# Optimization experiments

Hardware: AMD Instinct MI355X
Metric: run time of the kernel (lower is better)

The kernel has to match this reference:

```python
import jax, jax.numpy as jnp
import numpy as np
import math

V, D, L, M, S, B = 32000, 1024, 4, 4096, 2048, 4


def sinusoidal_positional_encoding(max_seq_len, embedding_dim):
    position = jnp.arange(max_seq_len, dtype=jnp.float32)[:, None]
    div_term = jnp.exp(jnp.arange(0, embedding_dim, 2, dtype=jnp.float32)
                       * (-math.log(10000.0) / embedding_dim))
    pe = jnp.zeros((max_seq_len, embedding_dim), jnp.float32)
    pe = pe.at[:, 0::2].set(jnp.sin(position * div_term))
    pe = pe.at[:, 1::2].set(jnp.cos(position * div_term))
    return pe


def setup_inputs() -> dict:
    key = jax.random.key(0)
    ks = jax.random.split(key, 12)
    s = 0.02
    return {
        "x": jax.random.randint(ks[0], (B, S), 0, V, dtype=jnp.int64),
        "emb": jax.random.normal(ks[1], (V, D), jnp.float32) * s,
        "pos_enc": sinusoidal_positional_encoding(S, D),
        "wq": jax.random.normal(ks[2], (D, D), jnp.float32) * s,
        "bq": jnp.zeros((D,), jnp.float32),
        "wk": jax.random.normal(ks[3], (D, D), jnp.float32) * s,
        "bk": jnp.zeros((D,), jnp.float32),
        "wv": jax.random.normal(ks[4], (D, D), jnp.float32) * s,
        "bv": jnp.zeros((D,), jnp.float32),
        "w1s": jax.random.normal(ks[5], (L, D, M), jnp.float32) * s,
        "b1s": jnp.zeros((L, M), jnp.float32),
        "w2s": jax.random.normal(ks[6], (L, M, D), jnp.float32) * s,
        "b2s": jnp.zeros((L, D), jnp.float32),
    }


def reference(x, emb, pos_enc, wq, bq, wk, bk, wv, bv, w1s, b1s, w2s, b2s):
    seq = x.shape[1]
    h = emb[x] + pos_enc[:seq]                      # [B,S,D]
    q = h @ wq + bq
    k = h @ wk + bk
    v = h @ wv + bv
    scores = jnp.einsum('bqd,bkd->bqk', q, k) / jnp.sqrt(jnp.float32(k.shape[-1]))
    # Faithful to source: triu(diagonal=0) KEPT -> attends to self and future.
    mask = jnp.triu(jnp.ones((seq, seq), bool), k=0)
    scores = jnp.where(mask, scores, -jnp.inf)
    attn = jax.nn.softmax(scores, axis=-1)
    h = jax.nn.relu(jnp.einsum('bqk,bkd->bqd', attn, v))
    for i in range(w1s.shape[0]):
        h = jax.nn.relu(h @ w1s[i] + b1s[i])
        h = jax.nn.relu(h @ w2s[i] + b2s[i])
    return h
```

## Files before the change

### kernel.cpp

```cpp
#include <hip/hip_runtime.h>

#define D_DIM 1024
#define S_DIM 2048
#define B_DIM 4
#define M_DIM 4096
#define NTOK  8192

typedef unsigned short u16;
typedef __attribute__((ext_vector_type(8))) short short8;
typedef __attribute__((ext_vector_type(4))) float fx4;

static __device__ __forceinline__ float b2f(u16 u) {
  union { unsigned int i; float f; } v; v.i = ((unsigned int)u) << 16; return v.f;
}
static __device__ __forceinline__ u16 f2b(float f) {
  union { float f; unsigned int i; } v; v.f = f;
  unsigned int r = v.i + 0x7fffu + ((v.i >> 16) & 1u);
  return (u16)(r >> 16);
}
static __device__ __forceinline__ void async16(u16* lds, const u16* g) {
  __builtin_amdgcn_global_load_lds(
      (__attribute__((address_space(1))) void*)(u16*)g,
      (__attribute__((address_space(3))) void*)lds, 16, 0, 0);
}

__global__ void canary_kernel(float* __restrict__ out) {
  const long i = ((long)blockIdx.x * 256 + threadIdx.x) * 4;
  float4 v = {1.0f, 1.0f, 1.0f, 1.0f};
  *(float4*)(out + i) = v;
}

__global__ void Transformer_33792802685820_kernel(
    const int* __restrict__ x, const float* __restrict__ emb,
    const float* __restrict__ pe, u16* __restrict__ h) {
  const int t = blockIdx.x;
  const int s = t & (S_DIM - 1);
  const int row = x[t];
  const int d = threadIdx.x * 4;
  float4 e = *(const float4*)(emb + (long)row * D_DIM + d);
  float4 p = *(const float4*)(pe + (long)s * D_DIM + d);
  ushort4 o;
  o.x = f2b(e.x + p.x);
  o.y = f2b(e.y + p.y);
  o.z = f2b(e.z + p.z);
  o.w = f2b(e.w + p.w);
  *(ushort4*)(h + (long)t * D_DIM + d) = o;
}

__global__ void transpose_f_kernel(
    const float* __restrict__ in, u16* __restrict__ out, int R, int C) {
  __shared__ float tile[32][33];
  const int c0 = blockIdx.x * 32, r0 = blockIdx.y * 32;
  const int tx = threadIdx.x, ty = threadIdx.y;
  for (int i = ty; i < 32; i += 8)
    tile[i][tx] = in[(long)(r0 + i) * C + (c0 + tx)];
  __syncthreads();
  for (int i = ty; i < 32; i += 8)
    out[(long)(c0 + i) * R + (r0 + tx)] = f2b(tile[tx][i]);
}

__global__ void transpose_b_kernel(
    const u16* __restrict__ in, u16* __restrict__ out, int R, int C) {
  __shared__ u16 tile[32][33];
  const long zoff = (long)blockIdx.z * R * C;
  const int c0 = blockIdx.x * 32, r0 = blockIdx.y * 32;
  const int tx = threadIdx.x, ty = threadIdx.y;
  for (int i = ty; i < 32; i += 8)
    tile[i][tx] = in[zoff + (long)(r0 + i) * C + (c0 + tx)];
  __syncthreads();
  for (int i = ty; i < 32; i += 8)
    out[zoff + (long)(c0 + i) * R + (r0 + tx)] = tile[tx][i];
}

template<int BN, bool RELU, bool BIAS, bool OUTF32>
__global__ __launch_bounds__(512) void gemm256(
    const u16* __restrict__ A, const u16* __restrict__ Bt,
    const float* __restrict__ bias, u16* __restrict__ C, float* __restrict__ Cf,
    int M, int N, int K, float scale, long sA_, long sB_, long sC_) {
  static_assert(BN == 256 || BN == 128, "BN");
  constexpr int WN   = BN / 64;
  constexpr int WM   = 8 / WN;
  constexpr int MF   = 256 / (WM * 16);
  constexpr int NB_B = BN / 64;

  __shared__ u16 sA0[256 * 64];
  __shared__ u16 sA1[256 * 64];
  __shared__ u16 sB0[BN * 64];
  __shared__ u16 sB1[BN * 64];

  const int tid  = threadIdx.x;
  const int lane = tid & 63;
  const int wave = tid >> 6;
  const int quad = lane >> 4;
  const int l16  = lane & 15;
  const int wm   = wave / WN;
  const int wn   = wave % WN;

  const int gx  = gridDim.x;
  const int nwg = gx * gridDim.y;
  const int id0 = blockIdx.y * gx + blockIdx.x;
  const int cpx = nwg >> 3;
  const int sid = (id0 & 7) * cpx + (id0 >> 3);
  const int n0  = (sid % gx) * BN;
  const int m0  = (sid / gx) << 8;

  A  += (long)blockIdx.z * sA_;
  Bt += (long)blockIdx.z * sB_;

  const int srow = tid >> 3;
  const int pc   = tid & 7;
  const int lc   = pc ^ (srow & 7);
  const u16* gA0 = A  + (long)(m0 + srow) * K + lc * 8;
  const u16* gB0 = Bt + (long)(n0 + srow) * K + lc * 8;
  const int ldst = tid << 3;

  fx4 acc[MF][4] = {};

  const int NT = K >> 6;

#define STG(Sa, Sb, t) do { \
    const long ko_ = (long)(t) << 6; \
    _Pragma("unroll") for (int bb_ = 0; bb_ < 4; ++bb_) \
      async16(&Sa[bb_ * 4096 + ldst], gA0 + (long)(bb_ * 64) * K + ko_); \
    _Pragma("unroll") for (int bb_ = 0; bb_ < NB_B; ++bb_) \
      async16(&Sb[bb_ * 4096 + ldst], gB0 + (long)(bb_ * 64) * K + ko_); \
  } while (0)

#define HALF(Sa, Sb) do { \
    _Pragma("unroll") for (int ks_ = 0; ks_ < 2; ++ks_) { \
      const int cko_ = ((((ks_) << 2) | quad) ^ (l16 & 7)) << 3; \
      short8 ar_[MF], br_[4]; \
      _Pragma("unroll") for (int i_ = 0; i_ < MF; ++i_) { \
        const int r_ = wm * (MF * 16) + i_ * 16 + l16; \
        ar_[i_] = *(const short8*)&Sa[(r_ >> 6) * 4096 + (r_ & 63) * 64 + cko_]; \
      } \
      _Pragma("unroll") for (int n_ = 0; n_ < 4; ++n_) { \
        const int r_ = wn * 64 + n_ * 16 + l16; \
        br_[n_] = *(const short8*)&Sb[(r_ >> 6) * 4096 + (r_ & 63) * 64 + cko_]; \
      } \
      __builtin_amdgcn_s_setprio(1); \
      _Pragma("unroll") for (int i_ = 0; i_ < MF; ++i_) \
        _Pragma("unroll") for (int n_ = 0; n_ < 4; ++n_) \
          acc[i_][n_] = __builtin_amdgcn_mfma_f32_16x16x32_bf16( \
              ar_[i_], br_[n_], acc[i_][n_], 0, 0, 0); \
      __builtin_amdgcn_s_setprio(0); \
    } \
  } while (0)

#define TILE_END do { \
    __builtin_amdgcn_sched_barrier(0); \
    asm volatile("s_waitcnt vmcnt(0)"); \
    __builtin_amdgcn_s_barrier(); \
    __builtin_amdgcn_sched_barrier(0); \
  } while (0)

  STG(sA0, sB0, 0);
  TILE_END;

  for (int t = 0; t < NT; t += 2) {
    STG(sA1, sB1, t + 1);
    HALF(sA0, sB0);
    TILE_END;
    if (t + 2 < NT) STG(sA0, sB0, t + 2);
    HALF(sA1, sB1);
    TILE_END;
  }

  float bv[4];
  #pragma unroll
  for (int n = 0; n < 4; ++n)
    bv[n] = BIAS ? bias[n0 + wn * 64 + n * 16 + l16] : 0.0f;

  #pragma unroll
  for (int f = 0; f < MF; ++f) {
    #pragma unroll
    for (int r = 0; r < 4; ++r) {
      const long row  = m0 + wm * (MF * 16) + f * 16 + quad * 4 + r;
      const long base = (long)blockIdx.z * sC_ + row * N + n0 + wn * 64 + l16;
      #pragma unroll
      for (int n = 0; n < 4; ++n) {
        float v = acc[f][n][r] * scale + bv[n];
        if (RELU) { if (v < 0.0f) v = 0.0f; }
        if (OUTF32) Cf[base + n * 16] = v;
        else        C [base + n * 16] = f2b(v);
      }
    }
  }
#undef STG
#undef HALF
#undef TILE_END
}

__global__ void softmax_kernel(u16* __restrict__ P) {
  const int q = blockIdx.x;
  u16* p = P + ((long)blockIdx.y * S_DIM + q) * S_DIM;
  const int tid = threadIdx.x;
  const int wave = tid >> 6, lane = tid & 63;
  __shared__ float red[4];
  float vals[8];
  float mx = -3.0e38f;
  for (int it = 0; it < 8; ++it) {
    int k = tid + it * 256;
    float v = (k >= q) ? b2f(p[k]) : -3.0e38f;
    vals[it] = v;
    mx = fmaxf(mx, v);
  }
  for (int off = 32; off > 0; off >>= 1)
    mx = fmaxf(mx, __shfl_down(mx, off, 64));
  if (lane == 0) red[wave] = mx;
  __syncthreads();
  mx = fmaxf(fmaxf(red[0], red[1]), fmaxf(red[2], red[3]));
  __syncthreads();
  float sum = 0.0f;
  for (int it = 0; it < 8; ++it) {
    int k = tid + it * 256;
    float e = (k >= q) ? __expf(vals[it] - mx) : 0.0f;
    vals[it] = e;
    sum += e;
  }
  for (int off = 32; off > 0; off >>= 1)
    sum += __shfl_down(sum, off, 64);
  if (lane == 0) red[wave] = sum;
  __syncthreads();
  sum = red[0] + red[1] + red[2] + red[3];
  const float inv = 1.0f / sum;
  for (int it = 0; it < 8; ++it) {
    int k = tid + it * 256;
    p[k] = f2b(vals[it] * inv);
  }
}

extern "C" void kernel_launch(void* const* d_in, const int* in_sizes, int n_in,
                              void* d_out, int out_size, void* d_ws, size_t ws_size,
                              hipStream_t stream) {
  (void)in_sizes; (void)n_in; (void)out_size; (void)ws_size;
  const int*   x   = (const int*)d_in[0];
  const float* emb = (const float*)d_in[1];
  const float* pe  = (const float*)d_in[2];
  const float* wq  = (const float*)d_in[3];
  const float* bq  = (const float*)d_in[4];
  const float* wk  = (const float*)d_in[5];
  const float* bk  = (const float*)d_in[6];
  const float* wv  = (const float*)d_in[7];
  const float* bv  = (const float*)d_in[8];
  const float* w1s = (const float*)d_in[9];
  const float* b1s = (const float*)d_in[10];
  const float* w2s = (const float*)d_in[11];
  const float* b2s = (const float*)d_in[12];
  float* out = (float*)d_out;

  u16* ws  = (u16*)d_ws;
  u16* h   = ws;
  u16* q   = h  + (long)NTOK * D_DIM;
  u16* kx  = q  + (long)NTOK * D_DIM;
  u16* v   = kx + (long)NTOK * D_DIM;
  u16* P   = v  + (long)NTOK * D_DIM;
  u16* wqT = P  + (long)B_DIM * S_DIM * S_DIM;
  u16* wkT = wqT + (long)D_DIM * D_DIM;
  u16* wvT = wkT + (long)D_DIM * D_DIM;
  u16* w1T = wvT + (long)D_DIM * D_DIM;
  u16* w2T = w1T + (long)D_DIM * M_DIM;
  u16* vT  = q;
  u16* mb  = kx;

  const dim3 blk256(256);
  const dim3 blk512(512);
  const dim3 blkT(32, 8);

  canary_kernel<<<dim3(NTOK), blk256, 0, stream>>>(out);

  transpose_f_kernel<<<dim3(32, 32), blkT, 0, stream>>>(wq, wqT, 1024, 1024);
  transpose_f_kernel<<<dim3(32, 32), blkT, 0, stream>>>(wk, wkT, 1024, 1024);
  transpose_f_kernel<<<dim3(32, 32), blkT, 0, stream>>>(wv, wvT, 1024, 1024);

  Transformer_33792802685820_kernel<<<dim3(NTOK), blk256, 0, stream>>>(x, emb, pe, h);

  gemm256<128, false, true, false><<<dim3(8, 32, 1), blk512, 0, stream>>>(h, wqT, bq, q,  nullptr, NTOK, D_DIM, D_DIM, 1.0f, 0, 0, 0);
  gemm256<128, false, true, false><<<dim3(8, 32, 1), blk512, 0, stream>>>(h, wkT, bk, kx, nullptr, NTOK, D_DIM, D_DIM, 1.0f, 0, 0, 0);
  gemm256<128, false, true, false><<<dim3(8, 32, 1), blk512, 0, stream>>>(h, wvT, bv, v,  nullptr, NTOK, D_DIM, D_DIM, 1.0f, 0, 0, 0);

  gemm256<256, false, false, false><<<dim3(8, 8, 4), blk512, 0, stream>>>(q, kx, nullptr, P, nullptr,
      S_DIM, S_DIM, D_DIM, 0.03125f, (long)S_DIM * D_DIM, (long)S_DIM * D_DIM, (long)S_DIM * S_DIM);

  softmax_kernel<<<dim3(S_DIM, B_DIM), blk256, 0, stream>>>(P);

  transpose_b_kernel<<<dim3(32, 64, 4), blkT, 0, stream>>>(v, vT, 2048, 1024);
  gemm256<128, true, false, false><<<dim3(8, 8, 4), blk512, 0, stream>>>(P, vT, nullptr, h, nullptr,
      S_DIM, D_DIM, S_DIM, 1.0f, (long)S_DIM * S_DIM, (long)D_DIM * S_DIM, (long)S_DIM * D_DIM);

  for (int i = 0; i < 4; ++i) {
    transpose_f_kernel<<<dim3(128, 32), blkT, 0, stream>>>(w1s + (long)i * D_DIM * M_DIM, w1T, 1024, 4096);
    transpose_f_kernel<<<dim3(32, 128), blkT, 0, stream>>>(w2s + (long)i * D_DIM * M_DIM, w2T, 4096, 1024);
    gemm256<256, true, true, false><<<dim3(16, 32, 1), blk512, 0, stream>>>(
        h, w1T, b1s + i * M_DIM, mb, nullptr, NTOK, M_DIM, D_DIM, 1.0f, 0, 0, 0);
    if (i == 3)
      gemm256<128, true, true, true><<<dim3(8, 32, 1), blk512, 0, stream>>>(
          mb, w2T, b2s + i * D_DIM, nullptr, out, NTOK, D_DIM, M_DIM, 1.0f, 0, 0, 0);
    else
      gemm256<128, true, true, false><<<dim3(8, 32, 1), blk512, 0, stream>>>(
          mb, w2T, b2s + i * D_DIM, h, nullptr, NTOK, D_DIM, M_DIM, 1.0f, 0, 0, 0);
  }
}
```

Before: 1.269 ms.

## Replace GEMM with 256x256 tile kernel using fine-grained 8-phase LDS pipeline

Measured after the change: 1.192 ms. 1.07x faster.

```diff
diff --git a/kernel.cpp b/kernel.cpp
--- a/kernel.cpp
+++ b/kernel.cpp
@@ -72,98 +72,112 @@
     out[zoff + (long)(c0 + i) * R + (r0 + tx)] = tile[tx][i];
 }
 
-template<int BN, bool RELU, bool BIAS, bool OUTF32>
-__global__ __launch_bounds__(512) void gemm256(
+template<bool RELU, bool BIAS, bool OUTF32>
+__global__ __launch_bounds__(512) void gemm8p(
     const u16* __restrict__ A, const u16* __restrict__ Bt,
     const float* __restrict__ bias, u16* __restrict__ C, float* __restrict__ Cf,
     int M, int N, int K, float scale, long sA_, long sB_, long sC_) {
-  static_assert(BN == 256 || BN == 128, "BN");
-  constexpr int WN   = BN / 64;
-  constexpr int WM   = 8 / WN;
-  constexpr int MF   = 256 / (WM * 16);
-  constexpr int NB_B = BN / 64;
-
-  __shared__ u16 sA0[256 * 64];
-  __shared__ u16 sA1[256 * 64];
-  __shared__ u16 sB0[BN * 64];
-  __shared__ u16 sB1[BN * 64];
+  __shared__ u16 sA0[16384];
+  __shared__ u16 sA1[16384];
+  __shared__ u16 sB0[16384];
+  __shared__ u16 sB1[16384];
 
   const int tid  = threadIdx.x;
   const int lane = tid & 63;
   const int wave = tid >> 6;
   const int quad = lane >> 4;
   const int l16  = lane & 15;
-  const int wm   = wave / WN;
-  const int wn   = wave % WN;
+  const int wm   = wave >> 2;
+  const int wn   = wave & 3;
 
   const int gx  = gridDim.x;
   const int nwg = gx * gridDim.y;
   const int id0 = blockIdx.y * gx + blockIdx.x;
   const int cpx = nwg >> 3;
   const int sid = (id0 & 7) * cpx + (id0 >> 3);
-  const int n0  = (sid % gx) * BN;
+  const int n0  = (sid % gx) << 8;
   const int m0  = (sid / gx) << 8;
 
   A  += (long)blockIdx.z * sA_;
   Bt += (long)blockIdx.z * sB_;
 
-  const int srow = tid >> 3;
-  const int pc   = tid & 7;
-  const int lc   = pc ^ (srow & 7);
+  const int srow = tid >> 2;
+  const int pc   = tid & 3;
+  const int lc   = pc ^ (srow & 3);
   const u16* gA0 = A  + (long)(m0 + srow) * K + lc * 8;
   const u16* gB0 = Bt + (long)(n0 + srow) * K + lc * 8;
   const int ldst = tid << 3;
 
-  fx4 acc[MF][4] = {};
+  const int cko = ((quad ^ (l16 & 3)) << 3);
+  const int baA = wm * 4096 + l16 * 32 + cko;
+  const int baB = (wn >> 1) * 4096 + (((wn & 1) << 6) + l16) * 32 + cko;
+
+  fx4 acc[8][4] = {};
+  short8 ar[4], br[4];
 
   const int NT = K >> 6;
 
-#define STG(Sa, Sb, t) do { \
-    const long ko_ = (long)(t) << 6; \
-    _Pragma("unroll") for (int bb_ = 0; bb_ < 4; ++bb_) \
-      async16(&Sa[bb_ * 4096 + ldst], gA0 + (long)(bb_ * 64) * K + ko_); \
-    _Pragma("unroll") for (int bb_ = 0; bb_ < NB_B; ++bb_) \
-      async16(&Sb[bb_ * 4096 + ldst], gB0 + (long)(bb_ * 64) * K + ko_); \
-  } while (0)
-
-#define HALF(Sa, Sb) do { \
-    _Pragma("unroll") for (int ks_ = 0; ks_ < 2; ++ks_) { \
-      const int cko_ = ((((ks_) << 2) | quad) ^ (l16 & 7)) << 3; \
-      short8 ar_[MF], br_[4]; \
-      _Pragma("unroll") for (int i_ = 0; i_ < MF; ++i_) { \
-        const int r_ = wm * (MF * 16) + i_ * 16 + l16; \
-        ar_[i_] = *(const short8*)&Sa[(r_ >> 6) * 4096 + (r_ & 63) * 64 + cko_]; \
-      } \
-      _Pragma("unroll") for (int n_ = 0; n_ < 4; ++n_) { \
-        const int r_ = wn * 64 + n_ * 16 + l16; \
-        br_[n_] = *(const short8*)&Sb[(r_ >> 6) * 4096 + (r_ & 63) * 64 + cko_]; \
-      } \
-      __builtin_amdgcn_s_setprio(1); \
-      _Pragma("unroll") for (int i_ = 0; i_ < MF; ++i_) \
-        _Pragma("unroll") for (int n_ = 0; n_ < 4; ++n_) \
-          acc[i_][n_] = __builtin_amdgcn_mfma_f32_16x16x32_bf16( \
-              ar_[i_], br_[n_], acc[i_][n_], 0, 0, 0); \
-      __builtin_amdgcn_s_setprio(0); \
-    } \
-  } while (0)
-
-#define TILE_END do { \
-    __builtin_amdgcn_sched_barrier(0); \
-    asm volatile("s_waitcnt vmcnt(0)"); \
-    __builtin_amdgcn_s_barrier(); \
-    __builtin_amdgcn_sched_barrier(0); \
-  } while (0)
-
-  STG(sA0, sB0, 0);
-  TILE_END;
+#define STG_A(S, t, kk) do { \
+    const long ko_ = (long)(t) * 64 + (kk) * 32; \
+    async16(&S[(kk) * 8192 + ldst],        gA0 + ko_); \
+    async16(&S[(kk) * 8192 + 4096 + ldst], gA0 + (long)128 * K + ko_); \
+  } while (0)
+#define STG_B(S, t, kk) do { \
+    const long ko_ = (long)(t) * 64 + (kk) * 32; \
+    async16(&S[(kk) * 8192 + ldst],        gB0 + ko_); \
+    async16(&S[(kk) * 8192 + 4096 + ldst], gB0 + (long)128 * K + ko_); \
+  } while (0)
+#define RD_A(S, mh, kk) do { \
+    _Pragma("unroll") for (int i_ = 0; i_ < 4; ++i_) \
+      ar[i_] = *(const short8*)&S[(kk) * 8192 + baA + ((mh) * 64 + i_ * 16) * 32]; \
+  } while (0)
+#define RD_B(S, kk) do { \
+    _Pragma("unroll") for (int n_ = 0; n_ < 4; ++n_) \
+      br[n_] = *(const short8*)&S[(kk) * 8192 + baB + n_ * 512]; \
+  } while (0)
+#define MM(mh) do { \
+    __builtin_amdgcn_s_setprio(1); \
+    _Pragma("unroll") for (int i_ = 0; i_ < 4; ++i_) \
+      _Pragma("unroll") for (int n_ = 0; n_ < 4; ++n_) \
+        acc[(mh) * 4 + i_][n_] = __builtin_amdgcn_mfma_f32_16x16x32_bf16( \
+            ar[i_], br[n_], acc[(mh) * 4 + i_][n_], 0, 0, 0); \
+    __builtin_amdgcn_s_setprio(0); \
+  } while (0)
+#define BARR  __builtin_amdgcn_s_barrier()
+#define LGKM  asm volatile("s_waitcnt lgkmcnt(0)")
+#define VM6   asm volatile("s_waitcnt vmcnt(6)")
+#define VM0   asm volatile("s_waitcnt vmcnt(0)")
+
+  STG_B(sB0, 0, 0); STG_A(sA0, 0, 0); STG_B(sB0, 0, 1); STG_A(sA0, 0, 1);
+  STG_B(sB1, 1, 0); STG_A(sA1, 1, 0); STG_B(sB1, 1, 1);
+  VM6; BARR;
 
   for (int t = 0; t < NT; t += 2) {
-    STG(sA1, sB1, t + 1);
-    HALF(sA0, sB0);
-    TILE_END;
-    if (t + 2 < NT) STG(sA0, sB0, t + 2);
-    HALF(sA1, sB1);
-    TILE_END;
+    const bool more = (t + 2 < NT);
+    RD_A(sA0, 0, 0); RD_B(sB0, 0);
+    STG_A(sA1, t + 1, 1);
+    BARR; LGKM; MM(0);
+    RD_A(sA0, 1, 0);
+    if (more) STG_B(sB0, t + 2, 0);
+    BARR; LGKM; MM(1);
+    RD_A(sA0, 0, 1); RD_B(sB0, 1);
+    if (more) STG_A(sA0, t + 2, 0);
+    BARR; LGKM; MM(0);
+    RD_A(sA0, 1, 1);
+    if (more) { STG_B(sB0, t + 2, 1); VM6; } else { VM0; }
+    BARR; LGKM; MM(1);
+    RD_A(sA1, 0, 0); RD_B(sB1, 0);
+    if (more) STG_A(sA0, t + 2, 1);
+    BARR; LGKM; MM(0);
+    RD_A(sA1, 1, 0);
+    if (more) STG_B(sB1, t + 3, 0);
+    BARR; LGKM; MM(1);
+    RD_A(sA1, 0, 1); RD_B(sB1, 1);
+    if (more) STG_A(sA1, t + 3, 0);
+    BARR; LGKM; MM(0);
+    RD_A(sA1, 1, 1);
+    if (more) { STG_B(sB1, t + 3, 1); VM6; }
+    BARR; LGKM; MM(1);
   }
 
   float bv[4];
@@ -172,10 +186,10 @@
     bv[n] = BIAS ? bias[n0 + wn * 64 + n * 16 + l16] : 0.0f;
 
   #pragma unroll
-  for (int f = 0; f < MF; ++f) {
+  for (int f = 0; f < 8; ++f) {
     #pragma unroll
     for (int r = 0; r < 4; ++r) {
-      const long row  = m0 + wm * (MF * 16) + f * 16 + quad * 4 + r;
+      const long row  = m0 + wm * 128 + f * 16 + quad * 4 + r;
       const long base = (long)blockIdx.z * sC_ + row * N + n0 + wn * 64 + l16;
       #pragma unroll
       for (int n = 0; n < 4; ++n) {
@@ -186,9 +200,15 @@
       }
     }
   }
-#undef STG
-#undef HALF
-#undef TILE_END
+#undef STG_A
+#undef STG_B
+#undef RD_A
+#undef RD_B
+#undef MM
+#undef BARR
+#undef LGKM
+#undef VM6
+#undef VM0
 }
 
 __global__ void softmax_kernel(u16* __restrict__ P) {
@@ -275,29 +295,29 @@
 
   Transformer_33792802685820_kernel<<<dim3(NTOK), blk256, 0, stream>>>(x, emb, pe, h);
 
-  gemm256<128, false, true, false><<<dim3(8, 32, 1), blk512, 0, stream>>>(h, wqT, bq, q,  nullptr, NTOK, D_DIM, D_DIM, 1.0f, 0, 0, 0);
-  gemm256<128, false, true, false><<<dim3(8, 32, 1), blk512, 0, stream>>>(h, wkT, bk, kx, nullptr, NTOK, D_DIM, D_DIM, 1.0f, 0, 0, 0);
-  gemm256<128, false, true, false><<<dim3(8, 32, 1), blk512, 0, stream>>>(h, wvT, bv, v,  nullptr, NTOK, D_DIM, D_DIM, 1.0f, 0, 0, 0);
-
-  gemm256<256, false, false, false><<<dim3(8, 8, 4), blk512, 0, stream>>>(q, kx, nullptr, P, nullptr,
+  gemm8p<false, true, false><<<dim3(4, 32, 1), blk512, 0, stream>>>(h, wqT, bq, q,  nullptr, NTOK, D_DIM, D_DIM, 1.0f, 0, 0, 0);
+  gemm8p<false, true, false><<<dim3(4, 32, 1), blk512, 0, stream>>>(h, wkT, bk, kx, nullptr, NTOK, D_DIM, D_DIM, 1.0f, 0, 0, 0);
+  gemm8p<false, true, false><<<dim3(4, 32, 1), blk512, 0, stream>>>(h, wvT, bv, v,  nullptr, NTOK, D_DIM, D_DIM, 1.0f, 0, 0, 0);
+
+  gemm8p<false, false, false><<<dim3(8, 8, 4), blk512, 0, stream>>>(q, kx, nullptr, P, nullptr,
       S_DIM, S_DIM, D_DIM, 0.03125f, (long)S_DIM * D_DIM, (long)S_DIM * D_DIM, (long)S_DIM * S_DIM);
 
   softmax_kernel<<<dim3(S_DIM, B_DIM), blk256, 0, stream>>>(P);
 
   transpose_b_kernel<<<dim3(32, 64, 4), blkT, 0, stream>>>(v, vT, 2048, 1024);
-  gemm256<128, true, false, false><<<dim3(8, 8, 4), blk512, 0, stream>>>(P, vT, nullptr, h, nullptr,
+  gemm8p<true, false, false><<<dim3(4, 8, 4), blk512, 0, stream>>>(P, vT, nullptr, h, nullptr,
       S_DIM, D_DIM, S_DIM, 1.0f, (long)S_DIM * S_DIM, (long)D_DIM * S_DIM, (long)S_DIM * D_DIM);
 
   for (int i = 0; i < 4; ++i) {
     transpose_f_kernel<<<dim3(128, 32), blkT, 0, stream>>>(w1s + (long)i * D_DIM * M_DIM, w1T, 1024, 4096);
     transpose_f_kernel<<<dim3(32, 128), blkT, 0, stream>>>(w2s + (long)i * D_DIM * M_DIM, w2T, 4096, 1024);
-    gemm256<256, true, true, false><<<dim3(16, 32, 1), blk512, 0, stream>>>(
+    gemm8p<true, true, false><<<dim3(16, 32, 1), blk512, 0, stream>>>(
         h, w1T, b1s + i * M_DIM, mb, nullptr, NTOK, M_DIM, D_DIM, 1.0f, 0, 0, 0);
     if (i == 3)
-      gemm256<128, true, true, true><<<dim3(8, 32, 1), blk512, 0, stream>>>(
+      gemm8p<true, true, true><<<dim3(4, 32, 1), blk512, 0, stream>>>(
           mb, w2T, b2s + i * D_DIM, nullptr, out, NTOK, D_DIM, M_DIM, 1.0f, 0, 0, 0);
     else
-      gemm256<128, true, true, false><<<dim3(8, 32, 1), blk512, 0, stream>>>(
+      gemm8p<true, true, false><<<dim3(4, 32, 1), blk512, 0, stream>>>(
           mb, w2T, b2s + i * D_DIM, h, nullptr, NTOK, D_DIM, M_DIM, 1.0f, 0, 0, 0);
   }
 }
```
